# Performance work log

Hardware: AMD Instinct MI355X
Metric: run time of the kernel (lower is better)

The kernel has to match this reference:

```python
import jax, jax.numpy as jnp
import numpy as np

UP = 8  # nn.Upsample(scale_factor=8), nearest


def _affine_grid(theta, H, W):
    # torch F.affine_grid, align_corners=False: pixel-center normalized coords
    xs = (jnp.arange(W, dtype=jnp.float32) + 0.5) * (2.0 / W) - 1.0
    ys = (jnp.arange(H, dtype=jnp.float32) + 0.5) * (2.0 / H) - 1.0
    base = jnp.stack([
        jnp.broadcast_to(xs[None, :], (H, W)),
        jnp.broadcast_to(ys[:, None], (H, W)),
        jnp.ones((H, W), jnp.float32),
    ], axis=-1)  # [H,W,3] = (x, y, 1)
    return jnp.einsum('hwk,bjk->bhwj', base, theta)  # [B,H,W,2], last dim = (x, y)


def _grid_sample(img, grid):
    # bilinear, padding_mode='zeros', align_corners=False (torch defaults)
    B, C, H, W = img.shape
    ix = ((grid[..., 0] + 1.0) * W - 1.0) * 0.5  # [B,Ho,Wo]
    iy = ((grid[..., 1] + 1.0) * H - 1.0) * 0.5
    ix0 = jnp.floor(ix)
    iy0 = jnp.floor(iy)
    wx1 = ix - ix0
    wy1 = iy - iy0

    def corner(xc, yc, w):
        valid = (xc >= 0) & (xc <= W - 1) & (yc >= 0) & (yc <= H - 1)
        xk = jnp.clip(xc, 0, W - 1).astype(jnp.int32)
        yk = jnp.clip(yc, 0, H - 1).astype(jnp.int32)
        g = jax.vmap(lambda im, yy, xx: im[:, yy, xx])(img, yk, xk)  # [B,C,Ho,Wo]
        return g * (w * valid.astype(img.dtype))[:, None, :, :]

    return (corner(ix0, iy0, (1.0 - wx1) * (1.0 - wy1))
            + corner(ix0 + 1.0, iy0, wx1 * (1.0 - wy1))
            + corner(ix0, iy0 + 1.0, (1.0 - wx1) * wy1)
            + corner(ix0 + 1.0, iy0 + 1.0, wx1 * wy1))


def setup_inputs() -> dict:
    key = jax.random.key(0)
    k1, k2 = jax.random.split(key)
    gt = jax.random.normal(k1, (8, 1, 128, 256), dtype=jnp.float32)
    theta = jax.random.normal(k2, (8, 6), dtype=jnp.float32)
    return {"gt": gt, "theta": theta, "output_sizex": 2048, "output_sizey": 1024}


def reference(gt, theta, output_sizex, output_sizey):
    onlyy = jnp.array([0., 0., 0., 0., 1., 1.], jnp.float32)
    offset = jnp.array([1., 0., 0., 0., 0., 0.], jnp.float32)
    thetay = (theta * onlyy + offset).reshape(-1, 2, 3)  # [[1,0,0],[0,t4,t5]]
    th = theta.reshape(-1, 2, 3)
    # nearest upsample x8
    gt_up = jnp.repeat(jnp.repeat(gt, UP, axis=2), UP, axis=3)
    grid = _affine_grid(th, output_sizey, output_sizex)
    box = _grid_sample(gt_up, grid)
    gridy = _affine_grid(thetay, output_sizey, output_sizex)
    boxy = _grid_sample(gt_up, gridy)
    return (box, boxy)
```

## Files before the change

### kernel.cpp

```cpp
#include <hip/hip_runtime.h>
#include <stdint.h>


#pragma clang fp contract(off)

constexpr int BATCH = 8;
constexpr int HI = 128, WI = 256;
constexpr int HO = 1024, WO = 2048;
constexpr size_t NPIX = (size_t)BATCH * HO * WO;

__global__ __launch_bounds__(256) void stn_kernel(
    const float* __restrict__ gt,
    const float* __restrict__ theta,
    float* __restrict__ out)
{
    const int row = blockIdx.x;
    const int b = row >> 10;
    const int h = row & (HO - 1);
    const int t = threadIdx.x;
    const int w0 = t << 3;

    const float* tb = theta + b * 6;
    const float t0 = tb[0], t1 = tb[1], t2 = tb[2];
    const float t3 = tb[3], t4 = tb[4], t5 = tb[5];
    const float* __restrict__ gtb = gt + b * (HI * WI);

    const float ys = (h + 0.5f) * (2.0f / (float)HO) - 1.0f;

    {
        const float gy2 = t4 * ys + t5;
        const float iy = ((gy2 + 1.0f) * (float)HO - 1.0f) * 0.5f;
        const float fy = floorf(iy);
        const float wy = iy - fy;
        const float vy0 = (fy >= 0.0f && fy <= (float)(HO - 1)) ? 1.0f : 0.0f;
        const float vy1 = (fy >= -1.0f && fy <= (float)(HO - 2)) ? 1.0f : 0.0f;
        const int y0 = ((int)fminf(fmaxf(fy,        0.0f), (float)(HO - 1))) >> 3;
        const int y1 = ((int)fminf(fmaxf(fy + 1.0f, 0.0f), (float)(HO - 1))) >> 3;
        const float s0 = gtb[y0 * WI + t];
        const float s1 = gtb[y1 * WI + t];
        const float byv = s0 * ((1.0f - wy) * vy0) + s1 * (wy * vy1);
        const float4 vb = make_float4(byv, byv, byv, byv);
        float4* dst = reinterpret_cast<float4*>(out + NPIX + (size_t)row * WO + w0);
        dst[0] = vb;
        dst[1] = vb;
    }

    const float cgx = t1 * ys + t2;
    const float cgy = t4 * ys + t5;
    float px[8];
#pragma unroll
    for (int p = 0; p < 8; ++p) {
        const float xn = (float)(w0 + p) * (2.0f / (float)WO) + (1.0f / (float)WO - 1.0f);
        const float gx = t0 * xn + cgx;
        const float gy = t3 * xn + cgy;
        const float ix = ((gx + 1.0f) * (float)WO - 1.0f) * 0.5f;
        const float iy = ((gy + 1.0f) * (float)HO - 1.0f) * 0.5f;
        const float fx = floorf(ix), fy = floorf(iy);
        const float wx = ix - fx,    wy = iy - fy;
        const float wx0 = (1.0f - wx) * ((fx >=  0.0f && fx <= (float)(WO - 1)) ? 1.0f : 0.0f);
        const float wx1 = wx          * ((fx >= -1.0f && fx <= (float)(WO - 2)) ? 1.0f : 0.0f);
        const float wy0 = (1.0f - wy) * ((fy >=  0.0f && fy <= (float)(HO - 1)) ? 1.0f : 0.0f);
        const float wy1 = wy          * ((fy >= -1.0f && fy <= (float)(HO - 2)) ? 1.0f : 0.0f);
        const int x0 = ((int)fminf(fmaxf(fx,        0.0f), (float)(WO - 1))) >> 3;
        const int x1 = ((int)fminf(fmaxf(fx + 1.0f, 0.0f), (float)(WO - 1))) >> 3;
        const int y0 = ((int)fminf(fmaxf(fy,        0.0f), (float)(HO - 1))) >> 3;
        const int y1 = ((int)fminf(fmaxf(fy + 1.0f, 0.0f), (float)(HO - 1))) >> 3;
        const float* __restrict__ r0 = gtb + y0 * WI;
        const float* __restrict__ r1 = gtb + y1 * WI;
        px[p] = wy0 * (wx0 * r0[x0] + wx1 * r0[x1])
              + wy1 * (wx0 * r1[x0] + wx1 * r1[x1]);
    }
    float4* dst = reinterpret_cast<float4*>(out + (size_t)row * WO + w0);
    dst[0] = make_float4(px[0], px[1], px[2], px[3]);
    dst[1] = make_float4(px[4], px[5], px[6], px[7]);
}

extern "C" void kernel_launch(void* const* d_in, const int* in_sizes, int n_in,
                              void* d_out, int out_size, void* d_ws, size_t ws_size,
                              hipStream_t stream) {
    const float* gt    = (const float*)d_in[0];
    const float* theta = (const float*)d_in[1];
    float* out = (float*)d_out;
    stn_kernel<<<BATCH * HO, 256, 0, stream>>>(gt, theta, out);
}
```

Before: 173.7 us.

## Pad source image with zero border, step coordinates incrementally, use nontemporal stores

Adds a pre-pass that copies each input image into a zero-padded buffer in workspace, so the sampler can drop per-corner validity masks and use clamped integer indices into the padded image. Sample coordinates are now advanced incrementally per pixel instead of recomputed, and the bilinear blend uses a lerp form with FMAs, with fp-contract no longer disabled. Output stores become nontemporal vector stores to avoid cache pollution on this write-bound kernel. The cost is an extra kernel launch and small workspace traffic, plus possible floating-point deviation from the incremental coordinates and changed rounding.

```diff
diff --git a/kernel.cpp b/kernel.cpp
--- a/kernel.cpp
+++ b/kernel.cpp
@@ -2,16 +2,35 @@
 #include <stdint.h>
 
 
-#pragma clang fp contract(off)
+typedef float vfloat4 __attribute__((ext_vector_type(4)));
 
 constexpr int BATCH = 8;
 constexpr int HI = 128, WI = 256;
 constexpr int HO = 1024, WO = 2048;
 constexpr size_t NPIX = (size_t)BATCH * HO * WO;
+constexpr int PH = HI + 2;
+constexpr int PSTRIDE = 264;
+constexpr size_t PIMG = (size_t)PH * PSTRIDE;
+
+__global__ __launch_bounds__(256) void pad_kernel(
+    const float* __restrict__ gt, float* __restrict__ P)
+{
+    const int i = blockIdx.x * 256 + threadIdx.x;
+    if (i >= (int)(BATCH * PIMG)) return;
+    const int b  = i / (int)PIMG;
+    const int r  = i - b * (int)PIMG;
+    const int y  = r / PSTRIDE - 1;
+    const int x  = r - (r / PSTRIDE) * PSTRIDE - 1;
+    float v = 0.0f;
+    if (y >= 0 && y < HI && x >= 0 && x < WI)
+        v = gt[(size_t)b * HI * WI + y * WI + x];
+    P[i] = v;
+}
 
 __global__ __launch_bounds__(256) void stn_kernel(
     const float* __restrict__ gt,
     const float* __restrict__ theta,
+    const float* __restrict__ P,
     float* __restrict__ out)
 {
     const int row = blockIdx.x;
@@ -24,6 +43,7 @@
     const float t0 = tb[0], t1 = tb[1], t2 = tb[2];
     const float t3 = tb[3], t4 = tb[4], t5 = tb[5];
     const float* __restrict__ gtb = gt + b * (HI * WI);
+    const float* __restrict__ Pb  = P + (size_t)b * PIMG + PSTRIDE + 1;
 
     const float ys = (h + 0.5f) * (2.0f / (float)HO) - 1.0f;
 
@@ -39,40 +59,44 @@
         const float s0 = gtb[y0 * WI + t];
         const float s1 = gtb[y1 * WI + t];
         const float byv = s0 * ((1.0f - wy) * vy0) + s1 * (wy * vy1);
-        const float4 vb = make_float4(byv, byv, byv, byv);
-        float4* dst = reinterpret_cast<float4*>(out + NPIX + (size_t)row * WO + w0);
-        dst[0] = vb;
-        dst[1] = vb;
+        const vfloat4 vb = {byv, byv, byv, byv};
+        vfloat4* dst = reinterpret_cast<vfloat4*>(out + NPIX + (size_t)row * WO + w0);
+        __builtin_nontemporal_store(vb, dst);
+        __builtin_nontemporal_store(vb, dst + 1);
     }
 
-    const float cgx = t1 * ys + t2;
-    const float cgy = t4 * ys + t5;
+    const float xn0 = (w0 + 0.5f) * (2.0f / (float)WO) - 1.0f;
+    const float gx0 = t0 * xn0 + (t1 * ys + t2);
+    const float gy0 = t3 * xn0 + (t4 * ys + t5);
+    float ix = ((gx0 + 1.0f) * (float)WO - 1.0f) * 0.5f;
+    float iy = ((gy0 + 1.0f) * (float)HO - 1.0f) * 0.5f;
+    const float dix = t0;
+    const float diy = 0.5f * t3;
+
     float px[8];
 #pragma unroll
     for (int p = 0; p < 8; ++p) {
-        const float xn = (float)(w0 + p) * (2.0f / (float)WO) + (1.0f / (float)WO - 1.0f);
-        const float gx = t0 * xn + cgx;
-        const float gy = t3 * xn + cgy;
-        const float ix = ((gx + 1.0f) * (float)WO - 1.0f) * 0.5f;
-        const float iy = ((gy + 1.0f) * (float)HO - 1.0f) * 0.5f;
         const float fx = floorf(ix), fy = floorf(iy);
         const float wx = ix - fx,    wy = iy - fy;
-        const float wx0 = (1.0f - wx) * ((fx >=  0.0f && fx <= (float)(WO - 1)) ? 1.0f : 0.0f);
-        const float wx1 = wx          * ((fx >= -1.0f && fx <= (float)(WO - 2)) ? 1.0f : 0.0f);
-        const float wy0 = (1.0f - wy) * ((fy >=  0.0f && fy <= (float)(HO - 1)) ? 1.0f : 0.0f);
-        const float wy1 = wy          * ((fy >= -1.0f && fy <= (float)(HO - 2)) ? 1.0f : 0.0f);
-        const int x0 = ((int)fminf(fmaxf(fx,        0.0f), (float)(WO - 1))) >> 3;
-        const int x1 = ((int)fminf(fmaxf(fx + 1.0f, 0.0f), (float)(WO - 1))) >> 3;
-        const int y0 = ((int)fminf(fmaxf(fy,        0.0f), (float)(HO - 1))) >> 3;
-        const int y1 = ((int)fminf(fmaxf(fy + 1.0f, 0.0f), (float)(HO - 1))) >> 3;
-        const float* __restrict__ r0 = gtb + y0 * WI;
-        const float* __restrict__ r1 = gtb + y1 * WI;
-        px[p] = wy0 * (wx0 * r0[x0] + wx1 * r0[x1])
-              + wy1 * (wx0 * r1[x0] + wx1 * r1[x1]);
+        const int xi = (int)fx, yi = (int)fy;
+        const int cx0 = min(max(xi >> 3,       -1), WI);
+        const int cx1 = min(max((xi + 1) >> 3, -1), WI);
+        const int cy0 = min(max(yi >> 3,       -1), HI);
+        const int cy1 = min(max((yi + 1) >> 3, -1), HI);
+        const float* __restrict__ r0 = Pb + cy0 * PSTRIDE;
+        const float* __restrict__ r1 = Pb + cy1 * PSTRIDE;
+        const float a = r0[cx0], bb = r0[cx1];
+        const float c = r1[cx0], d  = r1[cx1];
+        const float h0 = fmaf(wx, bb - a, a);
+        const float h1 = fmaf(wx, d - c,  c);
+        px[p] = fmaf(wy, h1 - h0, h0);
+        ix += dix; iy += diy;
     }
-    float4* dst = reinterpret_cast<float4*>(out + (size_t)row * WO + w0);
-    dst[0] = make_float4(px[0], px[1], px[2], px[3]);
-    dst[1] = make_float4(px[4], px[5], px[6], px[7]);
+    vfloat4* dst = reinterpret_cast<vfloat4*>(out + (size_t)row * WO + w0);
+    const vfloat4 v0 = {px[0], px[1], px[2], px[3]};
+    const vfloat4 v1 = {px[4], px[5], px[6], px[7]};
+    __builtin_nontemporal_store(v0, dst);
+    __builtin_nontemporal_store(v1, dst + 1);
 }
 
 extern "C" void kernel_launch(void* const* d_in, const int* in_sizes, int n_in,
@@ -81,5 +105,9 @@
     const float* gt    = (const float*)d_in[0];
     const float* theta = (const float*)d_in[1];
     float* out = (float*)d_out;
-    stn_kernel<<<BATCH * HO, 256, 0, stream>>>(gt, theta, out);
+    float* P   = (float*)d_ws;
+
+    const int padN = (int)(BATCH * PIMG);
+    pad_kernel<<<(padN + 255) / 256, 256, 0, stream>>>(gt, P);
+    stn_kernel<<<BATCH * HO, 256, 0, stream>>>(gt, theta, P, out);
 }
```

Result: no change. 172.9 us (-0.4%).
